# Kernel tuning notes

Measured on AMD Instinct MI355X. Metric: run time of the kernel, lower is better.

## Reference

```python
import jax, jax.numpy as jnp
import numpy as np

ORDER = 63
CODEBOOK_SIZE = 256
MIN_DATA = 1
N_ITER = 5
EPS = 1e-05
PERTURB = 1e-05


def setup_inputs() -> dict:
    key = jax.random.key(0)
    x = jax.random.normal(key, (131072, ORDER + 1), dtype=jnp.float32)
    return {"x": x}


def _e_step(x, cb, T):
    # squared euclidean distances via gram trick: (T, curr)
    d2 = jnp.sum(x * x, 1)[:, None] - 2.0 * (x @ cb.T) + jnp.sum(cb * cb, 1)[None, :]
    idx = jnp.argmin(d2, axis=1)
    xq = cb[idx]
    dist = jnp.sum((x - xq) ** 2) / T
    return idx, dist


def _m_step(x, idx, curr, key):
    D = x.shape[1]
    ones = jnp.ones((x.shape[0],), x.dtype)
    n_data = jax.ops.segment_sum(ones, idx, num_segments=curr)        # histc
    mask = n_data >= MIN_DATA
    sums = jax.ops.segment_sum(x, idx, num_segments=curr)             # scatter_add
    cent = sums / jnp.maximum(n_data, 1.0)[:, None]
    m = jnp.argmax(n_data)
    r = jax.random.normal(key, (curr, D), x.dtype) * PERTURB
    nm = (~mask).astype(x.dtype)
    # empty clusters reseeded from the largest cluster, perturbed
    new = jnp.where(mask[:, None], cent, cent[m][None, :] - r)
    cnt = jnp.sum(nm)
    corr = jnp.sum(r * nm[:, None], axis=0) / jnp.maximum(cnt, 1.0)
    new = new.at[m].add(jnp.where(cnt > 0, corr, jnp.zeros_like(corr)))
    return new


def _lbg(x):
    T, D = x.shape
    K = CODEBOOK_SIZE
    codebook = jnp.full((K, D), 1e10, x.dtype).at[0].set(jnp.mean(x, axis=0))
    distance = jnp.asarray(jnp.inf, x.dtype)
    base = jax.random.key(42)
    curr = 1
    split = 0
    while curr * 2 <= K:  # static loop over log2(K) binary splits
        key_s = jax.random.fold_in(base, split)
        kr, kloop = jax.random.split(key_s)
        r = jax.random.normal(kr, (curr, D), x.dtype) * PERTURB
        codebook = codebook.at[curr:2 * curr].set(codebook[:curr] - r).at[:curr].add(r)
        curr *= 2
        prev = distance

        def body(carry, n, curr=curr):
            cb, prev_d, dist, done, key = carry
            idx, d_new = _e_step(x, cb, T)
            change = jnp.abs(prev_d - d_new)
            conv = (n > 0) & (change / (d_new + 1e-16) < EPS)
            key, sub = jax.random.split(key)
            cb_new = _m_step(x, idx, curr, sub)
            stop = done | conv
            cb_out = jnp.where(stop, cb, cb_new)        # skip m-step on convergence/break
            dist_out = jnp.where(done, dist, d_new)     # distance assigned before break
            prev_out = jnp.where(stop, prev_d, d_new)
            return (cb_out, prev_out, dist_out, stop, key), None

        carry0 = (codebook[:curr], prev, distance, jnp.asarray(False), kloop)
        (cb_fin, _, distance, _, _), _ = jax.lax.scan(body, carry0, jnp.arange(N_ITER))
        codebook = codebook.at[:curr].set(cb_fin)
        split += 1
    return codebook, distance


def reference(x):
    return _lbg(x)
```

## Files before the change

### kernel.cpp

```cpp
#include <hip/hip_runtime.h>
#include <stdint.h>


#define NPTS 131072
#define DIMS 64
#define KCB  256
#define NCB  16

struct LbgState { float dist; float prev; unsigned int done; unsigned int k0, k1; unsigned int pad; };

__device__ __forceinline__ uint32_t rotl32(uint32_t v, int n){ return (v<<n)|(v>>(32-n)); }

__device__ __forceinline__ void tf2x32(uint32_t k0, uint32_t k1, uint32_t x0, uint32_t x1,
                                       uint32_t& o0, uint32_t& o1){
  uint32_t ks2 = k0 ^ k1 ^ 0x1BD11BDAu;
  x0 += k0; x1 += k1;
  #define TFR(r) { x0 += x1; x1 = rotl32(x1, r); x1 ^= x0; }
  TFR(13) TFR(15) TFR(26) TFR(6)
  x0 += k1; x1 += ks2 + 1u;
  TFR(17) TFR(29) TFR(16) TFR(24)
  x0 += ks2; x1 += k0 + 2u;
  TFR(13) TFR(15) TFR(26) TFR(6)
  x0 += k0; x1 += k1 + 3u;
  TFR(17) TFR(29) TFR(16) TFR(24)
  x0 += k1; x1 += ks2 + 4u;
  TFR(13) TFR(15) TFR(26) TFR(6)
  x0 += ks2; x1 += k0 + 5u;
  #undef TFR
  o0 = x0; o1 = x1;
}

__device__ __forceinline__ float xla_erfinv_f32(float x){
  float w = -log1pf(-x*x);
  float p;
  if (w < 5.0f){
    w = w - 2.5f;
    p = 2.81022636e-08f;
    p = fmaf(p, w, 3.43273939e-07f);
    p = fmaf(p, w, -3.5233877e-06f);
    p = fmaf(p, w, -4.39150654e-06f);
    p = fmaf(p, w, 0.00021858087f);
    p = fmaf(p, w, -0.00125372503f);
    p = fmaf(p, w, -0.00417768164f);
    p = fmaf(p, w, 0.246640727f);
    p = fmaf(p, w, 1.50140941f);
  } else {
    w = sqrtf(w) - 3.0f;
    p = -0.000200214257f;
    p = fmaf(p, w, 0.000100950558f);
    p = fmaf(p, w, 0.00134934322f);
    p = fmaf(p, w, -0.00367342844f);
    p = fmaf(p, w, 0.00573950773f);
    p = fmaf(p, w, -0.0076224613f);
    p = fmaf(p, w, 0.00943887047f);
    p = fmaf(p, w, 1.00167406f);
    p = fmaf(p, w, 2.83297682f);
  }
  return p * x;
}

__device__ __forceinline__ float jax_normal_elem(uint32_t k0, uint32_t k1, uint32_t j){
  uint32_t o0, o1; tf2x32(k0, k1, 0u, j, o0, o1);
  uint32_t bits = o0 ^ o1;
  uint32_t fb = (bits >> 9) | 0x3f800000u;
  float f = __uint_as_float(fb) - 1.0f;
  const float lo = -0.99999994f;
  float u = f * 2.0f + lo;
  u = fmaxf(lo, u);
  return 1.41421356f * xla_erfinv_f32(u);
}

__device__ void do_split(float* __restrict__ cb, float* __restrict__ cnorm,
                         unsigned long long* __restrict__ sums,
                         unsigned int* __restrict__ ndata,
                         unsigned long long* __restrict__ distacc,
                         LbgState* __restrict__ st, int curr, int split, int t){
  __shared__ uint32_t kr0s, kr1s;
  if (t == 0){
    uint32_t ks0, ks1, a0, a1, b0, b1;
    tf2x32(0u, 42u, 0u, (uint32_t)split, ks0, ks1);
    tf2x32(ks0, ks1, 0u, 0u, a0, a1);
    tf2x32(ks0, ks1, 0u, 1u, b0, b1);
    kr0s = a0; kr1s = a1;
    st->k0 = b0; st->k1 = b1;
    st->prev = st->dist;
    st->done = 0u;
  }
  __syncthreads();
  const int n = curr * DIMS;
  for (int e = t; e < n; e += 256){
    int c = e >> 6, d = e & 63;
    float rv = jax_normal_elem(kr0s, kr1s, (uint32_t)e) * 1e-5f;
    float old = cb[c*DIMS + d];
    cb[(curr + c)*DIMS + d] = old - rv;
    cb[c*DIMS + d]          = old + rv;
  }
  __syncthreads();
  const int c2 = curr * 2;
  for (int c = t; c < c2; c += 256){
    float s = 0.f;
    for (int d = 0; d < DIMS; d++){ float vv = cb[c*DIMS+d]; s += vv*vv; }
    cnorm[c] = s;
  }
  for (int e = t; e < c2*DIMS; e += 256) sums[e] = 0ull;
  for (int c = t; c < c2; c += 256) ndata[c] = 0u;
  if (t == 0) *distacc = 0ull;
}

__global__ void mean_kernel(const float* __restrict__ x, unsigned long long* __restrict__ macc,
                            float* __restrict__ cb, float* __restrict__ cnorm,
                            unsigned long long* __restrict__ sums,
                            unsigned int* __restrict__ ndata,
                            unsigned long long* __restrict__ distacc,
                            LbgState* __restrict__ st, unsigned int* __restrict__ mcnt){
  __shared__ double part[256];
  __shared__ float stage[16*64];
  __shared__ int islast;
  const int t = threadIdx.x;
  const int d = t & 63;
  const int w = t >> 6;
  const size_t base = (size_t)blockIdx.x * 1024;
  const int lrow = t >> 4;
  const int lcol = (t & 15) * 4;

  const float4* xg = reinterpret_cast<const float4*>(x);
  float4 nxt = xg[((base + lrow) * DIMS + lcol) >> 2];
  double s = 0.0;
  for (int tt = 0; tt < 64; tt++){
    float4 cur = nxt;
    if (tt < 63)
      nxt = xg[((base + (tt+1)*16 + lrow) * DIMS + lcol) >> 2];
    __syncthreads();
    *reinterpret_cast<float4*>(&stage[lrow*DIMS + lcol]) = cur;
    __syncthreads();
    s += (double)stage[(w    )*DIMS + d];
    s += (double)stage[(w + 4)*DIMS + d];
    s += (double)stage[(w + 8)*DIMS + d];
    s += (double)stage[(w +12)*DIMS + d];
  }
  part[t] = s;
  __syncthreads();
  if (t < 64){
    double tot = part[t] + part[64+t] + part[128+t] + part[192+t];
    atomicAdd(&macc[t], (unsigned long long)__double2ll_rn(tot * 1099511627776.0));
  }
  __threadfence();
  __syncthreads();
  if (t == 0) islast = (atomicAdd(mcnt, 1u) == (unsigned)(gridDim.x - 1));
  __syncthreads();
  if (!islast) return;

  if (t < 64){
    long long mv = (long long)atomicAdd(&macc[t], 0ull);
    double mean = (double)mv * (1.0/1099511627776.0) / 131072.0;
    cb[t] = (float)mean;
  }
  for (int e = t; e < KCB*DIMS; e += 256)
    if (e >= 64) cb[e] = 1e10f;
  if (t == 0){
    st->dist = __builtin_inff();
    st->prev = __builtin_inff();
    st->done = 0u;
    atomicExch(mcnt, 0u);
  }
  __syncthreads();
  do_split(cb, cnorm, sums, ndata, distacc, st, 1, 0, t);
}

template<int CURR>
__global__ __launch_bounds__(256, 4)
void estep_kernel(const float* __restrict__ x, const float* __restrict__ cb,
                  const float* __restrict__ cnorm, unsigned char* __restrict__ bidx8,
                  unsigned long long* __restrict__ distacc, const LbgState* __restrict__ st){
  if (st->done) return;
  const int t = threadIdx.x;
  const int lane = t & 63;
  const int p = blockIdx.x * 256 + t;

  float xv[DIMS];
  const float4* xp = reinterpret_cast<const float4*>(x + (size_t)p * DIMS);
  #pragma unroll
  for (int i = 0; i < 16; i++){
    float4 v = xp[i];
    xv[4*i+0] = v.x; xv[4*i+1] = v.y; xv[4*i+2] = v.z; xv[4*i+3] = v.w;
  }
  float xx = 0.f;
  #pragma unroll
  for (int d = 0; d < DIMS; d++) xx += xv[d] * xv[d];

  constexpr int NJ = (CURR < 4) ? CURR : 4;
  float best = __builtin_inff();
  int bi = 0;
  for (int j0 = 0; j0 < CURR; j0 += NJ){
    const float* crow = cb + (size_t)j0 * DIMS;
    float acc[NJ];
    #pragma unroll
    for (int k = 0; k < NJ; k++) acc[k] = 0.f;
    #pragma unroll
    for (int d = 0; d < DIMS; d++){
      #pragma unroll
      for (int k = 0; k < NJ; k++)
        acc[k] = fmaf(xv[d], crow[k*DIMS + d], acc[k]);
    }
    #pragma unroll
    for (int k = 0; k < NJ; k++){
      float d2 = (xx - 2.0f*acc[k]) + cnorm[j0 + k];
      if (d2 < best){ best = d2; bi = j0 + k; }
    }
  }
  bidx8[p] = (unsigned char)bi;

  double dd = 0.0;
  const float4* cbv = reinterpret_cast<const float4*>(cb + (size_t)bi * DIMS);
  #pragma unroll
  for (int i = 0; i < 16; i++){
    float4 b = cbv[i];
    float df, sq;
    df = xv[4*i+0] - b.x; sq = df*df; dd += (double)sq;
    df = xv[4*i+1] - b.y; sq = df*df; dd += (double)sq;
    df = xv[4*i+2] - b.z; sq = df*df; dd += (double)sq;
    df = xv[4*i+3] - b.w; sq = df*df; dd += (double)sq;
  }
  for (int off = 32; off > 0; off >>= 1) dd += __shfl_down(dd, off);
  if (lane == 0)
    atomicAdd(distacc, (unsigned long long)__double2ll_rn(dd * 4294967296.0));
}

template<int CURR>
__global__ __launch_bounds__(256, 3)
void estep_rx2(const float* __restrict__ x, const float* __restrict__ cb,
               const float* __restrict__ cnorm, unsigned char* __restrict__ bidx8,
               unsigned long long* __restrict__ distacc, const LbgState* __restrict__ st){
  if (st->done) return;
  constexpr int CPW = CURR / 4;
  constexpr int UNR = (CPW >= 4) ? 4 : CPW;
  __shared__ float4 xs[16*64];
  __shared__ float sbest[4*64];
  __shared__ int   sidx [4*64];
  const int t = threadIdx.x;
  const int lane = t & 63;
  const int w = __builtin_amdgcn_readfirstlane(t >> 6);
  const int pbase = blockIdx.x * 64;

  {
    const float4* xg = reinterpret_cast<const float4*>(x) + (size_t)pbase * 16;
    #pragma unroll
    for (int j = 0; j < 4; j++){
      const int q = t + 256*j;
      const int p = q >> 4, i = q & 15;
      xs[i*64 + p] = xg[q];
    }
  }
  __syncthreads();

  float4 xa[16];
  #pragma unroll
  for (int i = 0; i < 16; i++) xa[i] = xs[i*64 + lane];

  float xx0 = 0.f;
  #pragma unroll
  for (int i = 0; i < 16; i++){
    xx0 = fmaf(xa[i].x, xa[i].x, xx0); xx0 = fmaf(xa[i].y, xa[i].y, xx0);
    xx0 = fmaf(xa[i].z, xa[i].z, xx0); xx0 = fmaf(xa[i].w, xa[i].w, xx0);
  }

  float best0 = __builtin_inff();
  int bi0 = 0;
  const float4* cbg = reinterpret_cast<const float4*>(cb);
  const int cwbase = w * CPW;

  for (int cj = 0; cj < CPW; cj += UNR){
    float a0[UNR];
    #pragma unroll
    for (int u = 0; u < UNR; u++) a0[u] = 0.f;
    #pragma unroll
    for (int i = 0; i < 16; i++){
      #pragma unroll
      for (int u = 0; u < UNR; u++){
        float4 cf = cbg[(size_t)(cwbase + cj + u)*16 + i];
        a0[u] = fmaf(xa[i].x, cf.x, a0[u]); a0[u] = fmaf(xa[i].y, cf.y, a0[u]);
        a0[u] = fmaf(xa[i].z, cf.z, a0[u]); a0[u] = fmaf(xa[i].w, cf.w, a0[u]);
      }
    }
    #pragma unroll
    for (int u = 0; u < UNR; u++){
      float cn = cnorm[cwbase + cj + u];
      float d20 = (xx0 - 2.0f*a0[u]) + cn;
      if (d20 < best0){ best0 = d20; bi0 = cwbase + cj + u; }
    }
  }
  sbest[w*64 + lane] = best0;  sidx[w*64 + lane] = bi0;
  __syncthreads();

  if (t < 64){
    float best = sbest[t];
    int bi = sidx[t];
    #pragma unroll
    for (int ww = 1; ww < 4; ww++){
      float ob = sbest[ww*64 + t];
      int   oi = sidx [ww*64 + t];
      if (ob < best){ best = ob; bi = oi; }
    }
    bidx8[pbase + t] = (unsigned char)bi;
    const float4* cbv = cbg + (size_t)bi * 16;
    double dd = 0.0;
    #pragma unroll
    for (int i = 0; i < 16; i++){
      float4 xv = xa[i];
      float4 b = cbv[i];
      float df, sq;
      df = xv.x - b.x; sq = df*df; dd += (double)sq;
      df = xv.y - b.y; sq = df*df; dd += (double)sq;
      df = xv.z - b.z; sq = df*df; dd += (double)sq;
      df = xv.w - b.w; sq = df*df; dd += (double)sq;
    }
    for (int off = 32; off > 0; off >>= 1) dd += __shfl_down(dd, off);
    if ((t & 63) == 0)
      atomicAdd(distacc, (unsigned long long)__double2ll_rn(dd * 4294967296.0));
  }
}

template<int CURR, int NBLK>
__global__ __launch_bounds__(256)
void gather_kernel(const float* __restrict__ x, const unsigned char* __restrict__ bidx8,
                   unsigned long long* __restrict__ sums, unsigned int* __restrict__ ndata,
                   const LbgState* __restrict__ st){
  if (st->done) return;
  constexpr int CLOG = __builtin_ctz(CURR);
  constexpr int NCHUNK = NBLK / CURR;
  constexpr int PPC = NPTS / NCHUNK;
  constexpr int NPW = PPC / 4;
  __shared__ long long sacc[4][64][4];
  __shared__ unsigned int scw[4];
  const int t = threadIdx.x;
  const int lane = t & 63;
  const int w = t >> 6;
  const int c = blockIdx.x & (CURR - 1);
  const int chunk = blockIdx.x >> CLOG;
  const int pbase = chunk * PPC + w * NPW;
  const int sub = lane >> 4;
  const int dof = (lane & 15) * 4;

  long long a0 = 0, a1 = 0, a2 = 0, a3 = 0;
  unsigned int cnt = 0;
  int q0=0,q1=0,q2=0,q3=0,q4=0,q5=0,q6=0,q7=0, qn=0;
  const uint32_t* bp = reinterpret_cast<const uint32_t*>(bidx8 + pbase);
  for (int i = 0; i < NPW; i += 256){
    const uint32_t b4 = bp[(i >> 2) + lane];
    #pragma unroll
    for (int s = 0; s < 4; s++){
      unsigned long long m = __ballot(((b4 >> (8*s)) & 255u) == (unsigned)c);
      cnt += (unsigned int)__popcll(m);
      while (m){
        const int bit = __builtin_ctzll(m);
        m &= m - 1ull;
        const int p = pbase + i + bit*4 + s;
        if      (qn == 0) q0 = p;
        else if (qn == 1) q1 = p;
        else if (qn == 2) q2 = p;
        else if (qn == 3) q3 = p;
        else if (qn == 4) q4 = p;
        else if (qn == 5) q5 = p;
        else if (qn == 6) q6 = p;
        else              q7 = p;
        qn++;
        if (qn == 8){
          const int rA = (sub==0)?q0:(sub==1)?q1:(sub==2)?q2:q3;
          const int rB = (sub==0)?q4:(sub==1)?q5:(sub==2)?q6:q7;
          const float4 vA = *reinterpret_cast<const float4*>(x + (size_t)rA * DIMS + dof);
          const float4 vB = *reinterpret_cast<const float4*>(x + (size_t)rB * DIMS + dof);
          a0 += (long long)__double2int_rn((double)vA.x * 1048576.0);
          a1 += (long long)__double2int_rn((double)vA.y * 1048576.0);
          a2 += (long long)__double2int_rn((double)vA.z * 1048576.0);
          a3 += (long long)__double2int_rn((double)vA.w * 1048576.0);
          a0 += (long long)__double2int_rn((double)vB.x * 1048576.0);
          a1 += (long long)__double2int_rn((double)vB.y * 1048576.0);
          a2 += (long long)__double2int_rn((double)vB.z * 1048576.0);
          a3 += (long long)__double2int_rn((double)vB.w * 1048576.0);
          qn = 0;
        }
      }
    }
  }
  if (qn > 0){
    const int i1 = (qn > 1) ? q1 : q0;
    const int i2 = (qn > 2) ? q2 : q0;
    const int i3 = (qn > 3) ? q3 : q0;
    const int i4 = (qn > 4) ? q4 : q0;
    const int i5 = (qn > 5) ? q5 : q0;
    const int i6 = (qn > 6) ? q6 : q0;
    const int rA = (sub==0)?q0:(sub==1)?i1:(sub==2)?i2:i3;
    const int rB = (sub==0)?i4:(sub==1)?i5:(sub==2)?i6:q0;
    const float4 vA = *reinterpret_cast<const float4*>(x + (size_t)rA * DIMS + dof);
    const float4 vB = *reinterpret_cast<const float4*>(x + (size_t)rB * DIMS + dof);
    if (sub < qn){
      a0 += (long long)__double2int_rn((double)vA.x * 1048576.0);
      a1 += (long long)__double2int_rn((double)vA.y * 1048576.0);
      a2 += (long long)__double2int_rn((double)vA.z * 1048576.0);
      a3 += (long long)__double2int_rn((double)vA.w * 1048576.0);
    }
    if (sub + 4 < qn){
      a0 += (long long)__double2int_rn((double)vB.x * 1048576.0);
      a1 += (long long)__double2int_rn((double)vB.y * 1048576.0);
      a2 += (long long)__double2int_rn((double)vB.z * 1048576.0);
      a3 += (long long)__double2int_rn((double)vB.w * 1048576.0);
    }
  }
  sacc[w][lane][0] = a0; sacc[w][lane][1] = a1;
  sacc[w][lane][2] = a2; sacc[w][lane][3] = a3;
  if (lane == 0) scw[w] = cnt;
  __syncthreads();
  if (w == 0){
    long long tot = 0;
    #pragma unroll
    for (int ww = 0; ww < 4; ww++)
      #pragma unroll
      for (int r = 0; r < 4; r++)
        tot += sacc[ww][r*16 + (lane >> 2)][lane & 3];
    if (tot) atomicAdd(&sums[c*DIMS + lane], (unsigned long long)(tot * 1048576ll));
    if (lane == 0){
      unsigned int ct = scw[0] + scw[1] + scw[2] + scw[3];
      if (ct) atomicAdd(&ndata[c], ct);
    }
  }
}

__global__ void control_kernel(float* __restrict__ cb, float* __restrict__ cnorm,
                               const unsigned long long* __restrict__ sums_in,
                               unsigned long long* __restrict__ sums_out,
                               const unsigned int* __restrict__ ndata_in,
                               unsigned int* __restrict__ ndata_out,
                               const unsigned long long* __restrict__ distacc_in,
                               unsigned long long* __restrict__ distacc_out,
                               const LbgState* __restrict__ st_in,
                               LbgState* __restrict__ st_out,
                               int curr, int n_iter, int next_split){
  __shared__ float cm[64];
  __shared__ int redv[256];
  __shared__ int redi[256];
  __shared__ int s_m, s_cnt;
  const int t = threadIdx.x;
  const int b = blockIdx.x;

  const unsigned int done0 = st_in->done;
  float d_new = 0.f;
  int stop = 1;
  uint32_t sub0 = 0, sub1 = 0, nk0 = 0, nk1 = 0;
  if (!done0){
    double ddv = (double)(long long)(*distacc_in) * (1.0/4294967296.0);
    float sf = (float)ddv;
    d_new = sf / 131072.0f;
    float change = fabsf(st_in->prev - d_new);
    int conv = (n_iter > 0) && (change / (d_new + 1e-16f) < 1e-5f);
    stop = conv;
    if (!conv){
      tf2x32(st_in->k0, st_in->k1, 0u, 0u, nk0, nk1);
      tf2x32(st_in->k0, st_in->k1, 0u, 1u, sub0, sub1);
    }
  }

  const int rpb = (curr + NCB - 1) / NCB;
  const int r0 = b * rpb;
  int r1 = r0 + rpb; if (r1 > curr) r1 = curr;

  if (!done0 && !stop){
    int v = (t < curr) ? (int)ndata_in[t] : -1;
    redv[t] = v; redi[t] = t;
    __syncthreads();
    for (int s = 128; s > 0; s >>= 1){
      if (t < s){
        if (redv[t+s] > redv[t] || (redv[t+s] == redv[t] && redi[t+s] < redi[t])){
          redv[t] = redv[t+s]; redi[t] = redi[t+s];
        }
      }
      __syncthreads();
    }
    if (t == 0) s_m = redi[0];
    __syncthreads();
    redv[t] = (t < curr && ndata_in[t] == 0u) ? 1 : 0;
    __syncthreads();
    for (int s = 128; s > 0; s >>= 1){
      if (t < s) redv[t] += redv[t+s];
      __syncthreads();
    }
    if (t == 0) s_cnt = redv[0];
    __syncthreads();
    const int m = s_m;
    const int cntE = s_cnt;

    if (t < 64){
      unsigned int nm_ = ndata_in[m]; if (nm_ < 1u) nm_ = 1u;
      double cd = (double)(long long)sums_in[m*DIMS + t] * (1.0/1099511627776.0) / (double)nm_;
      cm[t] = (float)cd;
    }
    __syncthreads();

    for (int e = r0*DIMS + t; e < r1*DIMS; e += 256){
      int cc = e >> 6, d = e & 63;
      if (cc == m) continue;
      float nv;
      unsigned int nd = ndata_in[cc];
      if (nd >= 1u){
        double cd = (double)(long long)sums_in[e] * (1.0/1099511627776.0) / (double)nd;
        nv = (float)cd;
      } else {
        float rv = jax_normal_elem(sub0, sub1, (uint32_t)e) * 1e-5f;
        nv = cm[d] - rv;
      }
      cb[e] = nv;
    }
    if (m >= r0 && m < r1 && t < 64){
      float add = 0.f;
      if (cntE > 0){
        float acc = 0.f;
        for (int cc = 0; cc < curr; cc++){
          if (ndata_in[cc] == 0u)
            acc += jax_normal_elem(sub0, sub1, (uint32_t)(cc*DIMS + t)) * 1e-5f;
        }
        add = acc / fmaxf((float)cntE, 1.0f);
      }
      cb[m*DIMS + t] = cm[t] + add;
    }
    __syncthreads();

    for (int cc = r0 + t; cc < r1; cc += 256){
      float s = 0.f;
      for (int d = 0; d < DIMS; d++){ float vv = cb[cc*DIMS+d]; s += vv*vv; }
      cnorm[cc] = s;
    }
  }

  const int rows_next = (n_iter == 4 && curr < KCB) ? 2*curr : curr;
  for (int e = b*256 + t; e < rows_next*DIMS; e += NCB*256) sums_out[e] = 0ull;
  for (int cc = b*256 + t; cc < rows_next; cc += NCB*256) ndata_out[cc] = 0u;
  if (b == 0 && t == 0) *distacc_out = 0ull;

  if (b == 0 && t == 0){
    const float fin_dist = done0 ? st_in->dist : d_new;
    LbgState ns;
    ns.dist = fin_dist;
    if (done0 || stop){
      ns.prev = st_in->prev; ns.done = 1u; ns.k0 = st_in->k0; ns.k1 = st_in->k1;
    } else {
      ns.prev = d_new; ns.done = 0u; ns.k0 = nk0; ns.k1 = nk1;
    }
    ns.pad = 0u;
    if (n_iter == 4){
      if (curr < KCB){
        uint32_t ks0, ks1, sa0, sa1, sb0, sb1;
        tf2x32(0u, 42u, 0u, (uint32_t)next_split, ks0, ks1);
        tf2x32(ks0, ks1, 0u, 0u, sa0, sa1);
        tf2x32(ks0, ks1, 0u, 1u, sb0, sb1);
        ns.k0 = sb0; ns.k1 = sb1;
        ns.prev = fin_dist;
        ns.done = 0u;
      } else {
        cb[KCB*DIMS] = fin_dist;
      }
    }
    *st_out = ns;
  }

  if (n_iter == 4 && curr < KCB){
    uint32_t ks0, ks1, kr0, kr1;
    tf2x32(0u, 42u, 0u, (uint32_t)next_split, ks0, ks1);
    tf2x32(ks0, ks1, 0u, 0u, kr0, kr1);
    __syncthreads();
    for (int e = r0*DIMS + t; e < r1*DIMS; e += 256){
      int cc = e >> 6, d = e & 63;
      float rv = jax_normal_elem(kr0, kr1, (uint32_t)e) * 1e-5f;
      float old = cb[e];
      cb[(curr + cc)*DIMS + d] = old - rv;
      cb[e]                    = old + rv;
    }
    __syncthreads();
    for (int cc = r0 + t; cc < r1; cc += 256){
      float s0 = 0.f, s1 = 0.f;
      for (int d = 0; d < DIMS; d++){
        float v0 = cb[cc*DIMS + d];        s0 += v0*v0;
        float v1 = cb[(curr+cc)*DIMS + d]; s1 += v1*v1;
      }
      cnorm[cc] = s0;
      cnorm[curr + cc] = s1;
    }
  }
}

extern "C" void kernel_launch(void* const* d_in, const int* in_sizes, int n_in,
                              void* d_out, int out_size, void* d_ws, size_t ws_size,
                              hipStream_t stream){
  const float* x = (const float*)d_in[0];
  float* cb = (float*)d_out;
  char* ws = (char*)d_ws;
  unsigned long long* sums0   = (unsigned long long*)(ws + 0);
  unsigned long long* sums1   = (unsigned long long*)(ws + 131072);
  unsigned long long* macc    = (unsigned long long*)(ws + 262144);
  unsigned long long* dist0   = (unsigned long long*)(ws + 262656);
  unsigned long long* dist1   = (unsigned long long*)(ws + 262664);
  LbgState* st0               = (LbgState*)(ws + 262672);
  LbgState* st1               = (LbgState*)(ws + 262704);
  unsigned int* nd0           = (unsigned int*)(ws + 262736);
  unsigned int* nd1           = (unsigned int*)(ws + 263760);
  float* cnorm                = (float*)(ws + 264784);
  unsigned char* bidx8        = (unsigned char*)(ws + 265808);
  unsigned int* mcnt          = (unsigned int*)(ws + 396880);

  unsigned long long* sums[2] = { sums0, sums1 };
  unsigned long long* dac[2]  = { dist0, dist1 };
  LbgState* st[2]             = { st0, st1 };
  unsigned int* nd[2]         = { nd0, nd1 };

  hipMemsetAsync(d_ws, 0, 396884, stream);
  mean_kernel<<<128, 256, 0, stream>>>(x, macc, cb, cnorm, sums0, nd0, dist0, st0, mcnt);

  int g = 0;
  for (int split = 0; split < 8; split++){
    const int curr = 2 << split;
    for (int n = 0; n < 5; n++){
      const int pi = g & 1, po = pi ^ 1;
      switch (curr){
        case 2:   estep_kernel<2>  <<<512,256,0,stream>>>(x,cb,cnorm,bidx8,dac[pi],st[pi]);
                  gather_kernel<2,256>   <<<256, 256,0,stream>>>(x,bidx8,sums[pi],nd[pi],st[pi]); break;
        case 4:   estep_kernel<4>  <<<512,256,0,stream>>>(x,cb,cnorm,bidx8,dac[pi],st[pi]);
                  gather_kernel<4,512>   <<<512, 256,0,stream>>>(x,bidx8,sums[pi],nd[pi],st[pi]); break;
        case 8:   estep_rx2<8>   <<<2048,256,0,stream>>>(x,cb,cnorm,bidx8,dac[pi],st[pi]);
                  gather_kernel<8,1024>  <<<1024,256,0,stream>>>(x,bidx8,sums[pi],nd[pi],st[pi]); break;
        case 16:  estep_rx2<16>  <<<2048,256,0,stream>>>(x,cb,cnorm,bidx8,dac[pi],st[pi]);
                  gather_kernel<16,2048> <<<2048,256,0,stream>>>(x,bidx8,sums[pi],nd[pi],st[pi]); break;
        case 32:  estep_rx2<32>  <<<2048,256,0,stream>>>(x,cb,cnorm,bidx8,dac[pi],st[pi]);
                  gather_kernel<32,2048> <<<2048,256,0,stream>>>(x,bidx8,sums[pi],nd[pi],st[pi]); break;
        case 64:  estep_rx2<64>  <<<2048,256,0,stream>>>(x,cb,cnorm,bidx8,dac[pi],st[pi]);
                  gather_kernel<64,2048> <<<2048,256,0,stream>>>(x,bidx8,sums[pi],nd[pi],st[pi]); break;
        case 128: estep_rx2<128> <<<2048,256,0,stream>>>(x,cb,cnorm,bidx8,dac[pi],st[pi]);
                  gather_kernel<128,2048><<<2048,256,0,stream>>>(x,bidx8,sums[pi],nd[pi],st[pi]); break;
        case 256: estep_rx2<256> <<<2048,256,0,stream>>>(x,cb,cnorm,bidx8,dac[pi],st[pi]);
                  gather_kernel<256,2048><<<2048,256,0,stream>>>(x,bidx8,sums[pi],nd[pi],st[pi]); break;
      }
      control_kernel<<<NCB, 256, 0, stream>>>(cb, cnorm,
          sums[pi], sums[po], nd[pi], nd[po], dac[pi], dac[po],
          st[pi], st[po], curr, n, split+1);
      g++;
    }
  }
}
```

Measured before the change: 2.962 ms.

## Stream point features from LDS instead of registers in E-step kernel

The E-step kernel no longer keeps each point's 64 features in registers. It re-reads them from LDS on every k-step, which frees registers so launch bounds can rise from 3 to 8 blocks per CU. The inner loop now accumulates up to 16 centroids per group, which gives more reuse of each LDS-loaded x chunk. The global load of x is also rearranged so each thread reads four contiguous float4s of one point. The cost is more LDS traffic per FMA and a larger accumulator array that could spill under the tighter register budget.

```diff
diff --git a/kernel.cpp b/kernel.cpp
--- a/kernel.cpp
+++ b/kernel.cpp
@@ -227,13 +227,14 @@
 }
 
 template<int CURR>
-__global__ __launch_bounds__(256, 3)
-void estep_rx2(const float* __restrict__ x, const float* __restrict__ cb,
-               const float* __restrict__ cnorm, unsigned char* __restrict__ bidx8,
-               unsigned long long* __restrict__ distacc, const LbgState* __restrict__ st){
+__global__ __launch_bounds__(256, 8)
+void estep_sw64(const float* __restrict__ x, const float* __restrict__ cb,
+                const float* __restrict__ cnorm, unsigned char* __restrict__ bidx8,
+                unsigned long long* __restrict__ distacc, const LbgState* __restrict__ st){
   if (st->done) return;
   constexpr int CPW = CURR / 4;
-  constexpr int UNR = (CPW >= 4) ? 4 : CPW;
+  constexpr int NJG = (CPW < 16) ? CPW : 16;
+  constexpr int NG = CPW / NJG;
   __shared__ float4 xs[16*64];
   __shared__ float sbest[4*64];
   __shared__ int   sidx [4*64];
@@ -243,25 +244,20 @@
   const int pbase = blockIdx.x * 64;
 
   {
-    const float4* xg = reinterpret_cast<const float4*>(x) + (size_t)pbase * 16;
-    #pragma unroll
-    for (int j = 0; j < 4; j++){
-      const int q = t + 256*j;
-      const int p = q >> 4, i = q & 15;
-      xs[i*64 + p] = xg[q];
-    }
-  }
-  __syncthreads();
-
-  float4 xa[16];
-  #pragma unroll
-  for (int i = 0; i < 16; i++) xa[i] = xs[i*64 + lane];
+    const int p = t & 63, h = t >> 6;
+    const float4* xg = reinterpret_cast<const float4*>(x) + (size_t)(pbase + p) * 16 + h * 4;
+    #pragma unroll
+    for (int j = 0; j < 4; j++)
+      xs[(h*4 + j)*64 + p] = xg[j];
+  }
+  __syncthreads();
 
   float xx0 = 0.f;
   #pragma unroll
-  for (int i = 0; i < 16; i++){
-    xx0 = fmaf(xa[i].x, xa[i].x, xx0); xx0 = fmaf(xa[i].y, xa[i].y, xx0);
-    xx0 = fmaf(xa[i].z, xa[i].z, xx0); xx0 = fmaf(xa[i].w, xa[i].w, xx0);
+  for (int k4 = 0; k4 < 16; k4++){
+    float4 v = xs[k4*64 + lane];
+    xx0 = fmaf(v.x, v.x, xx0); xx0 = fmaf(v.y, v.y, xx0);
+    xx0 = fmaf(v.z, v.z, xx0); xx0 = fmaf(v.w, v.w, xx0);
   }
 
   float best0 = __builtin_inff();
@@ -269,24 +265,27 @@
   const float4* cbg = reinterpret_cast<const float4*>(cb);
   const int cwbase = w * CPW;
 
-  for (int cj = 0; cj < CPW; cj += UNR){
-    float a0[UNR];
-    #pragma unroll
-    for (int u = 0; u < UNR; u++) a0[u] = 0.f;
-    #pragma unroll
-    for (int i = 0; i < 16; i++){
+  for (int g = 0; g < NG; g++){
+    const int c0 = cwbase + g*NJG;
+    float acc0[NJG];
+    #pragma unroll
+    for (int cj = 0; cj < NJG; cj++) acc0[cj] = 0.f;
+    for (int k4 = 0; k4 < 16; k4++){
+      float4 xf0 = xs[k4*64 + lane];
       #pragma unroll
-      for (int u = 0; u < UNR; u++){
-        float4 cf = cbg[(size_t)(cwbase + cj + u)*16 + i];
-        a0[u] = fmaf(xa[i].x, cf.x, a0[u]); a0[u] = fmaf(xa[i].y, cf.y, a0[u]);
-        a0[u] = fmaf(xa[i].z, cf.z, a0[u]); a0[u] = fmaf(xa[i].w, cf.w, a0[u]);
-      }
-    }
-    #pragma unroll
-    for (int u = 0; u < UNR; u++){
-      float cn = cnorm[cwbase + cj + u];
-      float d20 = (xx0 - 2.0f*a0[u]) + cn;
-      if (d20 < best0){ best0 = d20; bi0 = cwbase + cj + u; }
+      for (int cj = 0; cj < NJG; cj++){
+        float4 cf = cbg[(size_t)(c0 + cj)*16 + k4];
+        acc0[cj] = fmaf(xf0.x, cf.x, acc0[cj]);
+        acc0[cj] = fmaf(xf0.y, cf.y, acc0[cj]);
+        acc0[cj] = fmaf(xf0.z, cf.z, acc0[cj]);
+        acc0[cj] = fmaf(xf0.w, cf.w, acc0[cj]);
+      }
+    }
+    #pragma unroll
+    for (int cj = 0; cj < NJG; cj++){
+      float cn = cnorm[c0 + cj];
+      float d20 = (xx0 - 2.0f*acc0[cj]) + cn;
+      if (d20 < best0){ best0 = d20; bi0 = c0 + cj; }
     }
   }
   sbest[w*64 + lane] = best0;  sidx[w*64 + lane] = bi0;
@@ -305,9 +304,9 @@
     const float4* cbv = cbg + (size_t)bi * 16;
     double dd = 0.0;
     #pragma unroll
-    for (int i = 0; i < 16; i++){
-      float4 xv = xa[i];
-      float4 b = cbv[i];
+    for (int k4 = 0; k4 < 16; k4++){
+      float4 xv = xs[k4*64 + t];
+      float4 b = cbv[k4];
       float df, sq;
       df = xv.x - b.x; sq = df*df; dd += (double)sq;
       df = xv.y - b.y; sq = df*df; dd += (double)sq;
@@ -623,17 +622,17 @@
                   gather_kernel<2,256>   <<<256, 256,0,stream>>>(x,bidx8,sums[pi],nd[pi],st[pi]); break;
         case 4:   estep_kernel<4>  <<<512,256,0,stream>>>(x,cb,cnorm,bidx8,dac[pi],st[pi]);
                   gather_kernel<4,512>   <<<512, 256,0,stream>>>(x,bidx8,sums[pi],nd[pi],st[pi]); break;
-        case 8:   estep_rx2<8>   <<<2048,256,0,stream>>>(x,cb,cnorm,bidx8,dac[pi],st[pi]);
+        case 8:   estep_sw64<8>   <<<2048,256,0,stream>>>(x,cb,cnorm,bidx8,dac[pi],st[pi]);
                   gather_kernel<8,1024>  <<<1024,256,0,stream>>>(x,bidx8,sums[pi],nd[pi],st[pi]); break;
-        case 16:  estep_rx2<16>  <<<2048,256,0,stream>>>(x,cb,cnorm,bidx8,dac[pi],st[pi]);
+        case 16:  estep_sw64<16>  <<<2048,256,0,stream>>>(x,cb,cnorm,bidx8,dac[pi],st[pi]);
                   gather_kernel<16,2048> <<<2048,256,0,stream>>>(x,bidx8,sums[pi],nd[pi],st[pi]); break;
-        case 32:  estep_rx2<32>  <<<2048,256,0,stream>>>(x,cb,cnorm,bidx8,dac[pi],st[pi]);
+        case 32:  estep_sw64<32>  <<<2048,256,0,stream>>>(x,cb,cnorm,bidx8,dac[pi],st[pi]);
                   gather_kernel<32,2048> <<<2048,256,0,stream>>>(x,bidx8,sums[pi],nd[pi],st[pi]); break;
-        case 64:  estep_rx2<64>  <<<2048,256,0,stream>>>(x,cb,cnorm,bidx8,dac[pi],st[pi]);
+        case 64:  estep_sw64<64>  <<<2048,256,0,stream>>>(x,cb,cnorm,bidx8,dac[pi],st[pi]);
                   gather_kernel<64,2048> <<<2048,256,0,stream>>>(x,bidx8,sums[pi],nd[pi],st[pi]); break;
-        case 128: estep_rx2<128> <<<2048,256,0,stream>>>(x,cb,cnorm,bidx8,dac[pi],st[pi]);
+        case 128: estep_sw64<128> <<<2048,256,0,stream>>>(x,cb,cnorm,bidx8,dac[pi],st[pi]);
                   gather_kernel<128,2048><<<2048,256,0,stream>>>(x,bidx8,sums[pi],nd[pi],st[pi]); break;
-        case 256: estep_rx2<256> <<<2048,256,0,stream>>>(x,cb,cnorm,bidx8,dac[pi],st[pi]);
+        case 256: estep_sw64<256> <<<2048,256,0,stream>>>(x,cb,cnorm,bidx8,dac[pi],st[pi]);
                   gather_kernel<256,2048><<<2048,256,0,stream>>>(x,bidx8,sums[pi],nd[pi],st[pi]); break;
       }
       control_kernel<<<NCB, 256, 0, stream>>>(cb, cnorm,
```

After: 3.040 ms. 1.03x slower.
